# Performance work log

Measured on AMD Instinct MI355X. Metric: run time of the kernel, lower is better.

The kernel has to match this reference:

```python
import jax, jax.numpy as jnp
import numpy as np

B, L, D, H = 2, 2048, 768, 12
DH = D // H          # 64
DFF = 4 * D          # 3072
ALPHA = 0.25         # lorentz_alpha
BLEND = 0.5          # blend for FFN and MinkowskiLayerNorm (set via set_blend)
EPS = 1e-5
SCALE = float(np.sqrt(DH))


def setup_inputs() -> dict:
    key = jax.random.key(0)
    ks = jax.random.split(key, 14)
    w = lambda k, shape: jax.random.normal(k, shape, jnp.float32) * 0.02
    causal = jnp.tril(jnp.ones((L, L), bool))
    attention_mask = jnp.where(causal, 0.0, -1e9).astype(jnp.float32)[None, None]
    return {
        'x': jax.random.normal(ks[0], (B, L, D), jnp.float32),
        'attention_mask': attention_mask,
        'timelike_mask': jax.random.bernoulli(ks[1], 0.25, (D,)),
        'Wq': w(ks[2], (D, D)), 'Wk': w(ks[3], (D, D)),
        'Wv': w(ks[4], (D, D)), 'Wo': w(ks[5], (D, D)),
        'w1': w(ks[6], (DFF, D)), 'w2': w(ks[7], (D, DFF)),
        'w1_t': w(ks[8], (DFF // 2, D)), 'w2_t': w(ks[9], (D, DFF // 2)),
        'w1_s': w(ks[10], (DFF // 2, D)), 'w2_s': w(ks[11], (D, DFF // 2)),
        'n1_w': jnp.ones(D, jnp.float32), 'n1_b': jnp.zeros(D, jnp.float32),
        'n2_w': jnp.ones(D, jnp.float32), 'n2_b': jnp.zeros(D, jnp.float32),
    }


def _mink_norm(x, m, w, b):
    # Minkowski LayerNorm blended with standard LN (m: float timelike mask)
    mean = x.mean(-1, keepdims=True)
    xc = x - mean
    var = (xc * xc).mean(-1, keepdims=True)
    x_std = xc / jnp.sqrt(var + EPS)
    sq = xc * xc
    eta = (sq * (1.0 - m)).sum(-1, keepdims=True) - (sq * m).sum(-1, keepdims=True)
    x_eta = xc / jnp.sqrt(jnp.abs(eta) + EPS)
    xn = (1.0 - BLEND) * x_std + BLEND * x_eta
    return w * xn + b


def _attn(x, attention_mask, m, Wq, Wk, Wv, Wo):
    # (B,L,D) -> (B,H,L,DH)
    split = lambda t: t.reshape(B, L, H, DH).transpose(0, 2, 1, 3)
    Q = split(x @ Wq.T)
    K = split(x @ Wk.T)
    V = split(x @ Wv.T)
    scores = jnp.einsum('bhqd,bhkd->bhqk', Q, K) / SCALE
    # Minkowski timelike correction: per-head diagonal mask on Q
    m2 = m.reshape(H, DH)[None, :, None, :]          # (1,H,1,DH)
    Q_t = Q * m2
    q_norm = jnp.linalg.norm(Q, axis=-1, keepdims=True)
    qt_norm = jnp.linalg.norm(Q_t, axis=-1, keepdims=True)
    sf = jnp.where(qt_norm > 1e-6, q_norm / jnp.maximum(qt_norm, 1e-8), 0.0)
    time_inner = jnp.einsum('bhqd,bhkd->bhqk', Q_t * sf, K) / SCALE
    scores = scores - 2.0 * ALPHA * time_inner
    scores = scores + attention_mask
    aw = jax.nn.softmax(scores, axis=-1)
    out = jnp.einsum('bhqk,bhkd->bhqd', aw, V)
    out = out.transpose(0, 2, 1, 3).reshape(B, L, D)
    return out @ Wo.T


def _ffn(x, m, w1, w2, w1_t, w2_t, w1_s, w2_s):
    std_out = jax.nn.gelu(x @ w1.T, approximate=False) @ w2.T
    h_t = jax.nn.silu((x * m) @ w1_t.T) @ w2_t.T
    h_s = jax.nn.gelu((x * (1.0 - m)) @ w1_s.T, approximate=False) @ w2_s.T
    return (1.0 - BLEND) * std_out + BLEND * (h_t + h_s)


def reference(x, attention_mask, timelike_mask, Wq, Wk, Wv, Wo,
              w1, w2, w1_t, w2_t, w1_s, w2_s, n1_w, n1_b, n2_w, n2_b):
    m = timelike_mask.astype(jnp.float32)
    ao = _attn(_mink_norm(x, m, n1_w, n1_b), attention_mask, m, Wq, Wk, Wv, Wo)
    x = x + ao
    x = x + _ffn(_mink_norm(x, m, n2_w, n2_b), m, w1, w2, w1_t, w2_t, w1_s, w2_s)
    return x
```

## Files before the change

### kernel.cpp

```cpp
#include <hip/hip_runtime.h>


typedef unsigned short u16;
typedef __bf16 bfrag __attribute__((ext_vector_type(8)));
typedef float f32x4 __attribute__((ext_vector_type(4)));

#define MFMA(a, b, c) __builtin_amdgcn_mfma_f32_16x16x32_bf16(a, b, c, 0, 0, 0)
#define NEG_BIG (-30000.0f)
#define ASYNC16(g, l)                                                        \
  __builtin_amdgcn_global_load_lds(                                          \
      (const __attribute__((address_space(1))) unsigned int*)(g),            \
      (__attribute__((address_space(3))) unsigned int*)(l), 16, 0, 0)

__device__ __forceinline__ float bf2f(u16 u) {
  unsigned int v = ((unsigned int)u) << 16;
  float f; __builtin_memcpy(&f, &v, 4); return f;
}
__device__ __forceinline__ u16 f2bf(float f) {
  unsigned int v; __builtin_memcpy(&v, &f, 4);
  v += 0x7fffu + ((v >> 16) & 1u);
  return (u16)(v >> 16);
}
__device__ __forceinline__ bfrag ldfrag(const u16* p) {
  bfrag v; __builtin_memcpy(&v, p, 16); return v;
}

__device__ __forceinline__ int xcd_work_id() {
  const int nx = gridDim.x, ny = gridDim.y;
  const int nwg = nx * ny * gridDim.z;
  const int orig = blockIdx.x + nx * (blockIdx.y + ny * blockIdx.z);
  if (nwg & 7) return orig;
  return (orig & 7) * (nwg >> 3) + (orig >> 3);
}

__global__ __launch_bounds__(256) void mask_conv_k(const void* __restrict__ mask,
                                                   float* __restrict__ mfl) {
  __shared__ int msh;
  if (threadIdx.x == 0) msh = 0;
  __syncthreads();
  const unsigned int* w = (const unsigned int*)mask;
  if (threadIdx.x < 192) {
    const unsigned int v = w[threadIdx.x];
    if ((v & 0xFFFFu) == 0x3F80u) atomicOr(&msh, 4);
    else if (v == 0x3F800000u) atomicOr(&msh, 2);
    else if (v >= 2u) atomicOr(&msh, 1);
  }
  __syncthreads();
  const int m = msh;
  const int mode = (m & 4) ? 3 : (m & 2) ? 2 : (m & 1) ? 1 : 0;
  for (int i = threadIdx.x; i < 768; i += 256) {
    int b;
    if (mode == 3) b = ((const u16*)mask)[i] != 0;
    else if (mode == 2) b = ((const float*)mask)[i] != 0.0f;
    else if (mode == 1) b = ((const unsigned char*)mask)[i] != 0;
    else b = ((const int*)mask)[i] != 0;
    mfl[i] = (float)b;
  }
}

struct Segs {
  const void* src[14];
  int off[14];
  int n[14];
  int mmode[14];
};

__global__ __launch_bounds__(256) void convert_k(Segs segs, u16* __restrict__ dstb,
                                                 const float* __restrict__ mfl) {
  const int seg = blockIdx.y;
  const int n = segs.n[seg];
  const int mm = segs.mmode[seg];
  u16* dst = dstb + segs.off[seg];
  const float* src = (const float*)segs.src[seg];
  for (int i = (blockIdx.x * 256 + threadIdx.x) * 4; i < n; i += gridDim.x * 1024) {
    float4 v;
    __builtin_memcpy(&v, src + i, 16);
    if (mm) {
      const int k = i % 768;
      float m0 = mfl[k], m1 = mfl[k + 1], m2 = mfl[k + 2], m3 = mfl[k + 3];
      if (mm == 2) { m0 = 1.f - m0; m1 = 1.f - m1; m2 = 1.f - m2; m3 = 1.f - m3; }
      v.x *= m0; v.y *= m1; v.z *= m2; v.w *= m3;
    }
    dst[i] = f2bf(v.x); dst[i + 1] = f2bf(v.y);
    dst[i + 2] = f2bf(v.z); dst[i + 3] = f2bf(v.w);
  }
}

__global__ __launch_bounds__(256) void mink_norm_k(
    const float* __restrict__ X, const float* __restrict__ mf,
    const u16* __restrict__ w, const u16* __restrict__ bias,
    u16* __restrict__ Y, float* __restrict__ Xcopy) {
  __shared__ float red[8];
  const int row = blockIdx.x, tid = threadIdx.x;
  const int wid = tid >> 6, lane = tid & 63;
  const size_t roff = (size_t)row * 768;

  float xv[3], mv[3];
  int idx[3];
#pragma unroll
  for (int i = 0; i < 3; i++) {
    idx[i] = tid + i * 256;
    xv[i] = X[roff + idx[i]];
    mv[i] = mf[idx[i]];
  }
  if (Xcopy) {
#pragma unroll
    for (int i = 0; i < 3; i++) Xcopy[roff + idx[i]] = xv[i];
  }
  float s = xv[0] + xv[1] + xv[2];
#pragma unroll
  for (int o = 32; o >= 1; o >>= 1) s += __shfl_xor(s, o, 64);
  if (lane == 0) red[wid] = s;
  __syncthreads();
  const float mean = (red[0] + red[1] + red[2] + red[3]) * (1.0f / 768.0f);
  __syncthreads();

  float xc[3], ss = 0.0f, sm = 0.0f;
#pragma unroll
  for (int i = 0; i < 3; i++) {
    xc[i] = xv[i] - mean;
    ss += xc[i] * xc[i];
    sm += xc[i] * xc[i] * mv[i];
  }
#pragma unroll
  for (int o = 32; o >= 1; o >>= 1) {
    ss += __shfl_xor(ss, o, 64);
    sm += __shfl_xor(sm, o, 64);
  }
  if (lane == 0) { red[wid] = ss; red[4 + wid] = sm; }
  __syncthreads();
  const float sumsq = red[0] + red[1] + red[2] + red[3];
  const float summ = red[4] + red[5] + red[6] + red[7];
  const float var = sumsq * (1.0f / 768.0f);
  const float eta = sumsq - 2.0f * summ;
  const float rs = 1.0f / sqrtf(var + 1e-5f);
  const float re = 1.0f / sqrtf(fabsf(eta) + 1e-5f);

#pragma unroll
  for (int i = 0; i < 3; i++) {
    const float xn = xc[i] * 0.5f * (rs + re);
    Y[roff + idx[i]] = f2bf(bf2f(w[idx[i]]) * xn + bf2f(bias[idx[i]]));
  }
}

__global__ __launch_bounds__(256) void qcorr_k(u16* __restrict__ Q,
                                               const float* __restrict__ mf) {
  const int idx = blockIdx.x * 4 + (threadIdx.x >> 6);
  const int t = threadIdx.x & 63;
  const int h = idx % 12;
  const int bl = idx / 12;
  const size_t off = (size_t)bl * 768 + h * 64 + t;
  const float q = bf2f(Q[off]);
  const float m = mf[h * 64 + t];
  float q2 = q * q, qm2 = q * q * m;
#pragma unroll
  for (int o = 32; o >= 1; o >>= 1) {
    q2 += __shfl_xor(q2, o, 64);
    qm2 += __shfl_xor(qm2, o, 64);
  }
  const float qn = sqrtf(q2), qtn = sqrtf(qm2);
  const float sf = (qtn > 1e-6f) ? qn / fmaxf(qtn, 1e-8f) : 0.0f;
  Q[off] = f2bf(q * (1.0f - 0.5f * sf * m) * 0.125f);
}

__device__ __forceinline__ void gemm128_loop(
    const u16* __restrict__ Ab, const u16* __restrict__ Wb2,
    int K, int lda, int ldb, u16 (*As)[32], u16 (*Bs)[32], f32x4 acc[4][4]) {
  const int tid = threadIdx.x;
  const int wid = tid >> 6, lane = tid & 63;
  const int lr = lane & 15, lq = lane >> 4;
  const int srow = wid * 32 + (lane >> 2);
  const int scol = (lane & 3) * 8;
  const u16* ga0 = Ab + (size_t)srow * lda + scol;
  const u16* ga1 = Ab + (size_t)(srow + 16) * lda + scol;
  const u16* gb0 = Wb2 + (size_t)srow * ldb + scol;
  const u16* gb1 = Wb2 + (size_t)(srow + 16) * ldb + scol;
  const int wr = (wid >> 1) * 64, wc = (wid & 1) * 64;
  const int nt = K >> 5;

#define STAGE16(dbuf, k0)                                                    \
  {                                                                          \
    u16* _a0 = &As[(dbuf) * 128 + wid * 32][0];                              \
    u16* _a1 = &As[(dbuf) * 128 + wid * 32 + 16][0];                         \
    u16* _b0 = &Bs[(dbuf) * 128 + wid * 32][0];                              \
    u16* _b1 = &Bs[(dbuf) * 128 + wid * 32 + 16][0];                         \
    ASYNC16(ga0 + (k0), _a0);                                                \
    ASYNC16(ga1 + (k0), _a1);                                                \
    ASYNC16(gb0 + (k0), _b0);                                                \
    ASYNC16(gb1 + (k0), _b1);                                                \
  }

  STAGE16(0, 0);
  for (int t = 0; t < nt; ++t) {
    const int cur = t & 1;
    if (t + 1 < nt) {
      STAGE16(cur ^ 1, (t + 1) << 5);
      __builtin_amdgcn_sched_barrier(0);
      asm volatile("s_waitcnt vmcnt(4)" ::: "memory");
    } else {
      asm volatile("s_waitcnt vmcnt(0)" ::: "memory");
    }
    __builtin_amdgcn_s_barrier();
    __builtin_amdgcn_sched_barrier(0);
    bfrag af[4], bf4[4];
#pragma unroll
    for (int i = 0; i < 4; i++)
      af[i] = ldfrag(&As[cur * 128 + wr + i * 16 + lr][lq * 8]);
#pragma unroll
    for (int j = 0; j < 4; j++)
      bf4[j] = ldfrag(&Bs[cur * 128 + wc + j * 16 + lr][lq * 8]);
#pragma unroll
    for (int i = 0; i < 4; i++)
#pragma unroll
      for (int j = 0; j < 4; j++)
        acc[i][j] = MFMA(af[i], bf4[j], acc[i][j]);
    asm volatile("s_waitcnt lgkmcnt(0)" ::: "memory");
    __builtin_amdgcn_sched_barrier(0);
    __builtin_amdgcn_s_barrier();
  }
#undef STAGE16
}

struct GSeg { const u16* W; u16* C; int ldc; int nblk; int epi; };
struct GArgs { GSeg s[3]; };

__global__ __launch_bounds__(256) void gemm128_fused(
    const u16* __restrict__ A, int lda, int K, GArgs args) {
  __shared__ __align__(16) u16 As[256][32];
  __shared__ __align__(16) u16 Bs[256][32];
  const int w = xcd_work_id();
  int cb = w % gridDim.x, seg = 0;
  const int by = w / gridDim.x;
  while (cb >= args.s[seg].nblk) { cb -= args.s[seg].nblk; seg++; }
  const GSeg g = args.s[seg];
  const int rowb = by * 128, colb = cb * 128;
  f32x4 acc[4][4] = {};
  gemm128_loop(A + (size_t)rowb * lda, g.W + (size_t)colb * K, K, lda, K,
               As, Bs, acc);

  const int lane = threadIdx.x & 63, wid = threadIdx.x >> 6;
  const int lr = lane & 15, lq = lane >> 4;
  const int wr = (wid >> 1) * 64, wc = (wid & 1) * 64;
#pragma unroll
  for (int i = 0; i < 4; i++)
#pragma unroll
    for (int j = 0; j < 4; j++)
#pragma unroll
      for (int r = 0; r < 4; r++) {
        const int row = rowb + wr + i * 16 + lq * 4 + r;
        const int col = colb + wc + j * 16 + lr;
        float v = acc[i][j][r];
        if (g.epi == 2) v = 0.5f * v * (1.0f + erff(v * 0.70710678118654752f));
        else if (g.epi == 3) v = v / (1.0f + __expf(-v));
        g.C[(size_t)row * g.ldc + col] = f2bf(v);
      }
}

__global__ __launch_bounds__(256) void gemm128_wo_splitk(
    const u16* __restrict__ A, const u16* __restrict__ W,
    float* __restrict__ Out) {
  __shared__ __align__(16) u16 As[256][32];
  __shared__ __align__(16) u16 Bs[256][32];
  const int w = xcd_work_id();
  const int bx = w % gridDim.x;
  const int by = (w / gridDim.x) % gridDim.y;
  const int z = w / (gridDim.x * gridDim.y);
  const int rowb = by * 128, colb = bx * 128;
  f32x4 acc[4][4] = {};
  gemm128_loop(A + (size_t)rowb * 768 + z * 384,
               W + (size_t)colb * 768 + z * 384, 384, 768, 768, As, Bs, acc);

  const int lane = threadIdx.x & 63, wid = threadIdx.x >> 6;
  const int lr = lane & 15, lq = lane >> 4;
  const int wr = (wid >> 1) * 64, wc = (wid & 1) * 64;
#pragma unroll
  for (int i = 0; i < 4; i++)
#pragma unroll
    for (int j = 0; j < 4; j++)
#pragma unroll
      for (int r = 0; r < 4; r++) {
        const int row = rowb + wr + i * 16 + lq * 4 + r;
        const int col = colb + wc + j * 16 + lr;
        atomicAdd(&Out[(size_t)row * 768 + col], acc[i][j][r]);
      }
}

__global__ __launch_bounds__(256) void ffn2_splitk(
    const u16* __restrict__ H1, const u16* __restrict__ Ht,
    const u16* __restrict__ Hs, const u16* __restrict__ W2,
    const u16* __restrict__ W2t, const u16* __restrict__ W2s,
    float* __restrict__ Out) {
  __shared__ __align__(16) u16 As[256][32];
  __shared__ __align__(16) u16 Bs[256][32];
  const int w = xcd_work_id();
  const int bx = w % gridDim.x;
  const int by = (w / gridDim.x) % gridDim.y;
  const int z = w / (gridDim.x * gridDim.y);
  const int rowb = by * 128, colb = bx * 128;
  f32x4 acc[4][4] = {};
  if (z == 0)
    gemm128_loop(H1 + (size_t)rowb * 3072, W2 + (size_t)colb * 3072,
                 1536, 3072, 3072, As, Bs, acc);
  else if (z == 1)
    gemm128_loop(H1 + (size_t)rowb * 3072 + 1536,
                 W2 + (size_t)colb * 3072 + 1536,
                 1536, 3072, 3072, As, Bs, acc);
  else if (z == 2)
    gemm128_loop(Ht + (size_t)rowb * 1536, W2t + (size_t)colb * 1536,
                 1536, 1536, 1536, As, Bs, acc);
  else
    gemm128_loop(Hs + (size_t)rowb * 1536, W2s + (size_t)colb * 1536,
                 1536, 1536, 1536, As, Bs, acc);

  const int lane = threadIdx.x & 63, wid = threadIdx.x >> 6;
  const int lr = lane & 15, lq = lane >> 4;
  const int wr = (wid >> 1) * 64, wc = (wid & 1) * 64;
#pragma unroll
  for (int i = 0; i < 4; i++)
#pragma unroll
    for (int j = 0; j < 4; j++)
#pragma unroll
      for (int r = 0; r < 4; r++) {
        const int row = rowb + wr + i * 16 + lq * 4 + r;
        const int col = colb + wc + j * 16 + lr;
        atomicAdd(&Out[(size_t)row * 768 + col], 0.5f * acc[i][j][r]);
      }
}

__global__ __launch_bounds__(256) void flash_attn_k(
    const u16* __restrict__ Qc, const u16* __restrict__ Kb,
    const u16* __restrict__ Vb, u16* __restrict__ O,
    float* __restrict__ Pn, float* __restrict__ Ph) {
  __shared__ __align__(16) u16 Ks[64][40];
  __shared__ __align__(16) u16 Vt[64][72];
  __shared__ __align__(16) u16 Ps[4][16][72];
  const int tid = threadIdx.x, wid = tid >> 6, lane = tid & 63;
  const int lr = lane & 15, lq = lane >> 4;

  int bx = blockIdx.x, qt = 0, c = 0;
  for (int q = 31; q >= 0; --q) {
    const int nc = (q < 8) ? 1 : (q / 8 + 1);
    if (bx < nc) { qt = q; c = bx; break; }
    bx -= nc;
  }
  const int nt = qt + 1;
  const int t0 = c * 8;
  const int t1 = (t0 + 8 < nt) ? t0 + 8 : nt;

  const int qb = qt * 64;
  const int bh = blockIdx.y;
  const int b = bh / 12, h = bh % 12;
  const int q0 = qb + wid * 16;
  const size_t base = (size_t)b * 2048 * 768 + h * 64;

  bfrag aq[2];
  aq[0] = ldfrag(Qc + base + (size_t)(q0 + lr) * 768 + lq * 8);
  aq[1] = ldfrag(Qc + base + (size_t)(q0 + lr) * 768 + 32 + lq * 8);

  f32x4 o[4] = {};
  float mrow[4] = {NEG_BIG, NEG_BIG, NEG_BIG, NEG_BIG};
  float lrow[4] = {0.0f, 0.0f, 0.0f, 0.0f};

  const int krow = tid >> 3;
  const int kcol = (tid & 7) * 8;
  const int vkey = tid & 31;
  const int vdg = tid >> 5;

  const u16* kp = Kb + base + (size_t)(t0 * 64 + krow) * 768 + kcol;
  const u16* vp = Vb + base + (size_t)(t0 * 64 + vkey) * 768 + vdg * 8;

  uint4 kv0, kv1, vv0, vv1;
  __builtin_memcpy(&kv0, kp, 16);
  __builtin_memcpy(&kv1, kp + (size_t)32 * 768, 16);
  __builtin_memcpy(&vv0, vp, 16);
  __builtin_memcpy(&vv1, vp + (size_t)32 * 768, 16);

  for (int kt = t0; kt < t1; kt++) {
    __syncthreads();
    __builtin_memcpy(&Ks[krow][kcol], &kv0, 16);
    __builtin_memcpy(&Ks[krow + 32][kcol], &kv1, 16);
    {
      union { uint4 u; u16 s[8]; } a, b2;
      a.u = vv0; b2.u = vv1;
#pragma unroll
      for (int j = 0; j < 8; j++) {
        Vt[vdg * 8 + j][vkey] = a.s[j];
        Vt[vdg * 8 + j][vkey + 32] = b2.s[j];
      }
    }
    __syncthreads();
    if (kt + 1 < t1) {
      const size_t koff = (size_t)(kt + 1 - t0) * 64 * 768;
      __builtin_memcpy(&kv0, kp + koff, 16);
      __builtin_memcpy(&kv1, kp + koff + (size_t)32 * 768, 16);
      __builtin_memcpy(&vv0, vp + koff, 16);
      __builtin_memcpy(&vv1, vp + koff + (size_t)32 * 768, 16);
    }

    const int kbk = kt * 64;
    {
      f32x4 s4[4] = {};
#pragma unroll
      for (int kg = 0; kg < 2; kg++) {
#pragma unroll
        for (int cc = 0; cc < 4; cc++) {
          bfrag bk = ldfrag(&Ks[cc * 16 + lr][kg * 32 + lq * 8]);
          s4[cc] = MFMA(aq[kg], bk, s4[cc]);
        }
      }
#pragma unroll
      for (int r = 0; r < 4; r++) {
        const int q = q0 + lq * 4 + r;
        float v[4];
        float mx = NEG_BIG;
#pragma unroll
        for (int cc = 0; cc < 4; cc++) {
          v[cc] = (kbk + cc * 16 + lr > q) ? NEG_BIG : s4[cc][r];
          mx = fmaxf(mx, v[cc]);
        }
#pragma unroll
        for (int off = 8; off >= 1; off >>= 1)
          mx = fmaxf(mx, __shfl_xor(mx, off, 16));
        const float mn = fmaxf(mrow[r], mx);
        const float alpha = __expf(mrow[r] - mn);
        float sm = 0.0f;
        float p[4];
#pragma unroll
        for (int cc = 0; cc < 4; cc++) {
          p[cc] = __expf(v[cc] - mn);
          sm += p[cc];
        }
#pragma unroll
        for (int off = 8; off >= 1; off >>= 1) sm += __shfl_xor(sm, off, 16);
        lrow[r] = lrow[r] * alpha + sm;
        mrow[r] = mn;
#pragma unroll
        for (int dt = 0; dt < 4; dt++) o[dt][r] *= alpha;
#pragma unroll
        for (int cc = 0; cc < 4; cc++)
          Ps[wid][lq * 4 + r][cc * 16 + lr] = f2bf(p[cc]);
      }
      __threadfence_block();
      bfrag pf0 = ldfrag(&Ps[wid][lr][lq * 8]);
      bfrag pf1 = ldfrag(&Ps[wid][lr][32 + lq * 8]);
#pragma unroll
      for (int dt = 0; dt < 4; dt++) {
        bfrag v0 = ldfrag(&Vt[dt * 16 + lr][lq * 8]);
        bfrag v1 = ldfrag(&Vt[dt * 16 + lr][32 + lq * 8]);
        o[dt] = MFMA(pf0, v0, o[dt]);
        o[dt] = MFMA(pf1, v1, o[dt]);
      }
    }
  }

  if (qt < 8) {
#pragma unroll
    for (int r = 0; r < 4; r++) {
      const float inv = 1.0f / fmaxf(lrow[r], 1e-30f);
      const int q = q0 + lq * 4 + r;
#pragma unroll
      for (int dt = 0; dt < 4; dt++)
        O[base + (size_t)q * 768 + dt * 16 + lr] = f2bf(o[dt][r] * inv);
    }
  } else {
    int off = 0;
    for (int j = 8; j < qt; ++j) off += j / 8 + 1;
    const int s = bh * 72 + off + c;
    float* Op = (s < 1536) ? Pn + (size_t)s * 4096
                           : Ph + (size_t)(s - 1536) * 4096;
    float* lmp = Ph + 786432 + (size_t)s * 128;
#pragma unroll
    for (int r = 0; r < 4; r++) {
      const int row = wid * 16 + lq * 4 + r;
#pragma unroll
      for (int dt = 0; dt < 4; dt++)
        Op[(size_t)row * 64 + dt * 16 + lr] = o[dt][r];
      if (lr == 0) { lmp[row] = mrow[r]; lmp[64 + row] = lrow[r]; }
    }
  }
}

__global__ __launch_bounds__(256) void attn_merge_k(
    const float* __restrict__ Pn, const float* __restrict__ Ph,
    u16* __restrict__ O) {
  const int qt = 8 + blockIdx.x;
  const int bh = blockIdx.y;
  const int b = bh / 12, h = bh % 12;
  const int nc = qt / 8 + 1;
  int off = 0;
  for (int j = 8; j < qt; ++j) off += j / 8 + 1;
  const int s0 = bh * 72 + off;
  const int row = threadIdx.x >> 2;
  const int c0 = (threadIdx.x & 3) * 16;
  const float* lmb = Ph + 786432;

  float mg = NEG_BIG;
  for (int cc = 0; cc < nc; ++cc)
    mg = fmaxf(mg, lmb[(size_t)(s0 + cc) * 128 + row]);

  float acc[16];
#pragma unroll
  for (int j = 0; j < 16; j++) acc[j] = 0.0f;
  float lg = 0.0f;
  for (int cc = 0; cc < nc; ++cc) {
    const int s = s0 + cc;
    const float mcv = lmb[(size_t)s * 128 + row];
    const float coef = __expf(mcv - mg);
    lg += coef * lmb[(size_t)s * 128 + 64 + row];
    const float* Op = (s < 1536) ? Pn + (size_t)s * 4096
                                 : Ph + (size_t)(s - 1536) * 4096;
    const float* rp = Op + (size_t)row * 64 + c0;
#pragma unroll
    for (int g = 0; g < 4; g++) {
      float4 v;
      __builtin_memcpy(&v, rp + g * 4, 16);
      acc[g * 4 + 0] += coef * v.x;
      acc[g * 4 + 1] += coef * v.y;
      acc[g * 4 + 2] += coef * v.z;
      acc[g * 4 + 3] += coef * v.w;
    }
  }
  const float inv = 1.0f / fmaxf(lg, 1e-30f);
  const int q = qt * 64 + row;
  const size_t ob = (size_t)b * 2048 * 768 + h * 64 + (size_t)q * 768 + c0;
#pragma unroll
  for (int j = 0; j < 16; j++) O[ob + j] = f2bf(acc[j] * inv);
}

extern "C" void kernel_launch(void* const* d_in, const int* in_sizes, int n_in,
                              void* d_out, int out_size, void* d_ws,
                              size_t ws_size, hipStream_t stream) {
  (void)in_sizes; (void)n_in; (void)out_size; (void)ws_size;
  const float* x = (const float*)d_in[0];
  const void* mask = d_in[2];

  char* ws = (char*)d_ws;
  u16* Wb  = (u16*)(ws);
  u16* n1h = (u16*)(ws + 23599104);
  u16* Qb  = (u16*)(ws + 48764928);
  u16* Kb2 = (u16*)(ws + 55056384);
  u16* Vb2 = (u16*)(ws + 61347840);
  u16* att = (u16*)(ws + 67639296);
  u16* hs  = (u16*)(ws + 80222208);
  float* mfl = (float*)(ws + 92805120);
  float* x1 = (float*)d_out;
  float* Pn = (float*)n1h;
  float* Ph = (float*)hs;

  u16* Wq = Wb + 0,        *Wk = Wb + 589824,   *Wv = Wb + 1179648;
  u16* Wo = Wb + 1769472,  *w1 = Wb + 2359296,  *w1t = Wb + 4718592;
  u16* w1s = Wb + 5898240, *w2 = Wb + 7077888,  *w2t = Wb + 9437184;
  u16* w2s = Wb + 10616832;
  u16* n1w = Wb + 11796480, *n1b = Wb + 11797248;
  u16* n2w = Wb + 11798016, *n2b = Wb + 11798784;

  Segs sg;
  const int srcidx[14] = {3, 4, 5, 6, 7, 9, 11, 8, 10, 12, 13, 14, 15, 16};
  const int offs[14] = {0, 589824, 1179648, 1769472, 2359296, 4718592,
                        5898240, 7077888, 9437184, 10616832,
                        11796480, 11797248, 11798016, 11798784};
  const int ns[14] = {589824, 589824, 589824, 589824, 2359296, 1179648,
                      1179648, 2359296, 1179648, 1179648, 768, 768, 768, 768};
  const int mms[14] = {0, 0, 0, 0, 0, 1, 2, 0, 0, 0, 0, 0, 0, 0};
  for (int i = 0; i < 14; i++) {
    sg.src[i] = d_in[srcidx[i]];
    sg.off[i] = offs[i];
    sg.n[i] = ns[i];
    sg.mmode[i] = mms[i];
  }

  mask_conv_k<<<1, 256, 0, stream>>>(mask, mfl);
  convert_k<<<dim3(2304, 14), 256, 0, stream>>>(sg, Wb, mfl);

  mink_norm_k<<<4096, 256, 0, stream>>>(x, mfl, n1w, n1b, n1h, x1);

  GArgs qkv;
  qkv.s[0] = {Wq, Qb, 768, 6, 0};
  qkv.s[1] = {Wk, Kb2, 768, 6, 0};
  qkv.s[2] = {Wv, Vb2, 768, 6, 0};
  gemm128_fused<<<dim3(18, 32), 256, 0, stream>>>(n1h, 768, 768, qkv);

  qcorr_k<<<12288, 256, 0, stream>>>(Qb, mfl);

  flash_attn_k<<<dim3(80, 24), 256, 0, stream>>>(Qb, Kb2, Vb2, att, Pn, Ph);
  attn_merge_k<<<dim3(24, 24), 256, 0, stream>>>(Pn, Ph, att);

  gemm128_wo_splitk<<<dim3(6, 32, 2), 256, 0, stream>>>(att, Wo, x1);

  mink_norm_k<<<4096, 256, 0, stream>>>(x1, mfl, n2w, n2b, Qb, nullptr);

  GArgs ffn1;
  ffn1.s[0] = {w1, n1h, 3072, 24, 2};
  ffn1.s[1] = {w1t, att, 1536, 12, 3};
  ffn1.s[2] = {w1s, hs, 1536, 12, 2};
  gemm128_fused<<<dim3(48, 32), 256, 0, stream>>>(Qb, 768, 768, ffn1);

  ffn2_splitk<<<dim3(6, 32, 4), 256, 0, stream>>>(n1h, att, hs, w2, w2t, w2s,
                                                  (float*)d_out);
}
```

Measured before the change: 424.2 us.

## Replace atomic split-K FFN2 with three-way partial buffers and a reduce kernel

The second FFN GEMM now uses a three-way split instead of four. The standard branch runs its full K=3072 and updates the output in place without atomics. The timelike and spacelike branches write their partials to scratch buffers, one in fp32 and one in bf16, and a new elementwise kernel adds them into the output. This removes roughly twelve million fp32 atomicAdds and remaps block order across XCDs. In exchange, the z=0 blocks do twice the K work of the others, so the load is uneven, and there is an extra kernel launch. Rounding the spacelike partial to bf16 also adds some error.

```diff
diff --git a/kernel.cpp b/kernel.cpp
--- a/kernel.cpp
+++ b/kernel.cpp
@@ -285,27 +285,24 @@
       }
 }
 
-__global__ __launch_bounds__(256) void ffn2_splitk(
+__global__ __launch_bounds__(256) void ffn2_split3(
     const u16* __restrict__ H1, const u16* __restrict__ Ht,
     const u16* __restrict__ Hs, const u16* __restrict__ W2,
     const u16* __restrict__ W2t, const u16* __restrict__ W2s,
-    float* __restrict__ Out) {
+    float* __restrict__ Out, float* __restrict__ Pt, u16* __restrict__ Ps16) {
   __shared__ __align__(16) u16 As[256][32];
   __shared__ __align__(16) u16 Bs[256][32];
-  const int w = xcd_work_id();
-  const int bx = w % gridDim.x;
-  const int by = (w / gridDim.x) % gridDim.y;
-  const int z = w / (gridDim.x * gridDim.y);
+  const int orig = blockIdx.x + 6 * (blockIdx.y + 32 * blockIdx.z);
+  const int w = (orig & 7) * 72 + (orig >> 3);
+  const int z = w % 3;
+  const int bx = (w / 3) % 6;
+  const int by = w / 18;
   const int rowb = by * 128, colb = bx * 128;
   f32x4 acc[4][4] = {};
   if (z == 0)
     gemm128_loop(H1 + (size_t)rowb * 3072, W2 + (size_t)colb * 3072,
-                 1536, 3072, 3072, As, Bs, acc);
+                 3072, 3072, 3072, As, Bs, acc);
   else if (z == 1)
-    gemm128_loop(H1 + (size_t)rowb * 3072 + 1536,
-                 W2 + (size_t)colb * 3072 + 1536,
-                 1536, 3072, 3072, As, Bs, acc);
-  else if (z == 2)
     gemm128_loop(Ht + (size_t)rowb * 1536, W2t + (size_t)colb * 1536,
                  1536, 1536, 1536, As, Bs, acc);
   else
@@ -323,8 +320,27 @@
       for (int r = 0; r < 4; r++) {
         const int row = rowb + wr + i * 16 + lq * 4 + r;
         const int col = colb + wc + j * 16 + lr;
-        atomicAdd(&Out[(size_t)row * 768 + col], 0.5f * acc[i][j][r]);
+        const size_t o = (size_t)row * 768 + col;
+        if (z == 0) Out[o] = Out[o] + 0.5f * acc[i][j][r];
+        else if (z == 1) Pt[o] = acc[i][j][r];
+        else Ps16[o] = f2bf(acc[i][j][r]);
       }
+}
+
+__global__ __launch_bounds__(256) void ffn2_reduce(
+    float* __restrict__ Out, const float* __restrict__ Pt,
+    const u16* __restrict__ Ps16) {
+  const int i = (blockIdx.x * 256 + threadIdx.x) * 4;
+  float4 o, t;
+  __builtin_memcpy(&o, Out + i, 16);
+  __builtin_memcpy(&t, Pt + i, 16);
+  ushort4 s;
+  __builtin_memcpy(&s, Ps16 + i, 8);
+  o.x += 0.5f * (t.x + bf2f(s.x));
+  o.y += 0.5f * (t.y + bf2f(s.y));
+  o.z += 0.5f * (t.z + bf2f(s.z));
+  o.w += 0.5f * (t.w + bf2f(s.w));
+  __builtin_memcpy(Out + i, &o, 16);
 }
 
 __global__ __launch_bounds__(256) void flash_attn_k(
@@ -546,6 +562,8 @@
   float* x1 = (float*)d_out;
   float* Pn = (float*)n1h;
   float* Ph = (float*)hs;
+  float* Pt = (float*)Qb;
+  u16* Ps16 = Vb2;
 
   u16* Wq = Wb + 0,        *Wk = Wb + 589824,   *Wv = Wb + 1179648;
   u16* Wo = Wb + 1769472,  *w1 = Wb + 2359296,  *w1t = Wb + 4718592;
@@ -595,6 +613,7 @@
   ffn1.s[2] = {w1s, hs, 1536, 12, 2};
   gemm128_fused<<<dim3(48, 32), 256, 0, stream>>>(Qb, 768, 768, ffn1);
 
-  ffn2_splitk<<<dim3(6, 32, 4), 256, 0, stream>>>(n1h, att, hs, w2, w2t, w2s,
-                                                  (float*)d_out);
-}
+  ffn2_split3<<<dim3(6, 32, 3), 256, 0, stream>>>(n1h, att, hs, w2, w2t, w2s,
+                                                  (float*)d_out, Pt, Ps16);
+  ffn2_reduce<<<3072, 256, 0, stream>>>((float*)d_out, Pt, Ps16);
+}
```

Result: slower. 438.2 us (+3.3%).

## Fuse Q timelike correction into QKV GEMM epilogue, finer attention split with fp16 partials

Applied to the files above, without the earlier changes.

Drops the separate qcorr kernel and instead computes the per-head Q norm and timelike-norm correction inside the QKV GEMM epilogue, using cross-lane shuffles over the 64-column head slice each wave owns. The flash attention split-KV chunk size goes from 8 to 4 KV tiles, which raises the block count and balances load across the causal triangle. Partial outputs are now stored as fp16 instead of fp32, with the max and sum statistics moved to a separate buffer. The fp16 partials halve the merge traffic but lose some precision, and the smaller chunks mean more partials to write and merge.

```diff
diff --git a/kernel.cpp b/kernel.cpp
--- a/kernel.cpp
+++ b/kernel.cpp
@@ -20,6 +20,12 @@
   unsigned int v; __builtin_memcpy(&v, &f, 4);
   v += 0x7fffu + ((v >> 16) & 1u);
   return (u16)(v >> 16);
+}
+__device__ __forceinline__ u16 f2h(float f) {
+  _Float16 h = (_Float16)f; u16 u; __builtin_memcpy(&u, &h, 2); return u;
+}
+__device__ __forceinline__ float h2f(u16 u) {
+  _Float16 h; __builtin_memcpy(&h, &u, 2); return (float)h;
 }
 __device__ __forceinline__ bfrag ldfrag(const u16* p) {
   bfrag v; __builtin_memcpy(&v, p, 16); return v;
@@ -143,26 +149,6 @@
   }
 }
 
-__global__ __launch_bounds__(256) void qcorr_k(u16* __restrict__ Q,
-                                               const float* __restrict__ mf) {
-  const int idx = blockIdx.x * 4 + (threadIdx.x >> 6);
-  const int t = threadIdx.x & 63;
-  const int h = idx % 12;
-  const int bl = idx / 12;
-  const size_t off = (size_t)bl * 768 + h * 64 + t;
-  const float q = bf2f(Q[off]);
-  const float m = mf[h * 64 + t];
-  float q2 = q * q, qm2 = q * q * m;
-#pragma unroll
-  for (int o = 32; o >= 1; o >>= 1) {
-    q2 += __shfl_xor(q2, o, 64);
-    qm2 += __shfl_xor(qm2, o, 64);
-  }
-  const float qn = sqrtf(q2), qtn = sqrtf(qm2);
-  const float sf = (qtn > 1e-6f) ? qn / fmaxf(qtn, 1e-8f) : 0.0f;
-  Q[off] = f2bf(q * (1.0f - 0.5f * sf * m) * 0.125f);
-}
-
 __device__ __forceinline__ void gemm128_loop(
     const u16* __restrict__ Ab, const u16* __restrict__ Wb2,
     int K, int lda, int ldb, u16 (*As)[32], u16 (*Bs)[32], f32x4 acc[4][4]) {
@@ -225,7 +211,8 @@
 struct GArgs { GSeg s[3]; };
 
 __global__ __launch_bounds__(256) void gemm128_fused(
-    const u16* __restrict__ A, int lda, int K, GArgs args) {
+    const u16* __restrict__ A, int lda, int K, GArgs args,
+    const float* __restrict__ mfl) {
   __shared__ __align__(16) u16 As[256][32];
   __shared__ __align__(16) u16 Bs[256][32];
   const int w = xcd_work_id();
@@ -241,6 +228,41 @@
   const int lane = threadIdx.x & 63, wid = threadIdx.x >> 6;
   const int lr = lane & 15, lq = lane >> 4;
   const int wr = (wid >> 1) * 64, wc = (wid & 1) * 64;
+
+  if (g.epi == 1) {
+    const int cb64 = colb + wc;
+    float mj[4];
+#pragma unroll
+    for (int j = 0; j < 4; j++) mj[j] = mfl[cb64 + j * 16 + lr];
+#pragma unroll
+    for (int i = 0; i < 4; i++)
+#pragma unroll
+      for (int r = 0; r < 4; r++) {
+        float p2 = 0.0f, pm2 = 0.0f;
+#pragma unroll
+        for (int j = 0; j < 4; j++) {
+          const float v = acc[i][j][r];
+          p2 += v * v;
+          pm2 += v * v * mj[j];
+        }
+#pragma unroll
+        for (int off = 8; off >= 1; off >>= 1) {
+          p2 += __shfl_xor(p2, off, 64);
+          pm2 += __shfl_xor(pm2, off, 64);
+        }
+        const float qn = sqrtf(p2), qtn = sqrtf(pm2);
+        const float sf = (qtn > 1e-6f) ? qn / fmaxf(qtn, 1e-8f) : 0.0f;
+        const int row = rowb + wr + i * 16 + lq * 4 + r;
+#pragma unroll
+        for (int j = 0; j < 4; j++) {
+          const int col = cb64 + j * 16 + lr;
+          const float v = acc[i][j][r] * (1.0f - 0.5f * sf * mj[j]) * 0.125f;
+          g.C[(size_t)row * g.ldc + col] = f2bf(v);
+        }
+      }
+    return;
+  }
+
 #pragma unroll
   for (int i = 0; i < 4; i++)
 #pragma unroll
@@ -330,7 +352,7 @@
 __global__ __launch_bounds__(256) void flash_attn_k(
     const u16* __restrict__ Qc, const u16* __restrict__ Kb,
     const u16* __restrict__ Vb, u16* __restrict__ O,
-    float* __restrict__ Pn, float* __restrict__ Ph) {
+    u16* __restrict__ Pn, u16* __restrict__ Ph, float* __restrict__ Lm) {
   __shared__ __align__(16) u16 Ks[64][40];
   __shared__ __align__(16) u16 Vt[64][72];
   __shared__ __align__(16) u16 Ps[4][16][72];
@@ -339,13 +361,13 @@
 
   int bx = blockIdx.x, qt = 0, c = 0;
   for (int q = 31; q >= 0; --q) {
-    const int nc = (q < 8) ? 1 : (q / 8 + 1);
+    const int nc = (q < 4) ? 1 : (q / 4 + 1);
     if (bx < nc) { qt = q; c = bx; break; }
     bx -= nc;
   }
   const int nt = qt + 1;
-  const int t0 = c * 8;
-  const int t1 = (t0 + 8 < nt) ? t0 + 8 : nt;
+  const int t0 = c * 4;
+  const int t1 = (t0 + 4 < nt) ? t0 + 4 : nt;
 
   const int qb = qt * 64;
   const int bh = blockIdx.y;
@@ -453,7 +475,7 @@
     }
   }
 
-  if (qt < 8) {
+  if (qt < 4) {
 #pragma unroll
     for (int r = 0; r < 4; r++) {
       const float inv = 1.0f / fmaxf(lrow[r], 1e-30f);
@@ -464,39 +486,38 @@
     }
   } else {
     int off = 0;
-    for (int j = 8; j < qt; ++j) off += j / 8 + 1;
-    const int s = bh * 72 + off + c;
-    float* Op = (s < 1536) ? Pn + (size_t)s * 4096
-                           : Ph + (size_t)(s - 1536) * 4096;
-    float* lmp = Ph + 786432 + (size_t)s * 128;
+    for (int j = 4; j < qt; ++j) off += j / 4 + 1;
+    const int s = bh * 140 + off + c;
+    u16* Op = (s < 3072) ? Pn + (size_t)s * 4096
+                         : Ph + (size_t)(s - 3072) * 4096;
+    float* lmp = Lm + (size_t)s * 128;
 #pragma unroll
     for (int r = 0; r < 4; r++) {
       const int row = wid * 16 + lq * 4 + r;
 #pragma unroll
       for (int dt = 0; dt < 4; dt++)
-        Op[(size_t)row * 64 + dt * 16 + lr] = o[dt][r];
+        Op[(size_t)row * 64 + dt * 16 + lr] = f2h(o[dt][r]);
       if (lr == 0) { lmp[row] = mrow[r]; lmp[64 + row] = lrow[r]; }
     }
   }
 }
 
 __global__ __launch_bounds__(256) void attn_merge_k(
-    const float* __restrict__ Pn, const float* __restrict__ Ph,
-    u16* __restrict__ O) {
-  const int qt = 8 + blockIdx.x;
+    const u16* __restrict__ Pn, const u16* __restrict__ Ph,
+    const float* __restrict__ Lm, u16* __restrict__ O) {
+  const int qt = 4 + blockIdx.x;
   const int bh = blockIdx.y;
   const int b = bh / 12, h = bh % 12;
-  const int nc = qt / 8 + 1;
+  const int nc = qt / 4 + 1;
   int off = 0;
-  for (int j = 8; j < qt; ++j) off += j / 8 + 1;
-  const int s0 = bh * 72 + off;
+  for (int j = 4; j < qt; ++j) off += j / 4 + 1;
+  const int s0 = bh * 140 + off;
   const int row = threadIdx.x >> 2;
   const int c0 = (threadIdx.x & 3) * 16;
-  const float* lmb = Ph + 786432;
 
   float mg = NEG_BIG;
   for (int cc = 0; cc < nc; ++cc)
-    mg = fmaxf(mg, lmb[(size_t)(s0 + cc) * 128 + row]);
+    mg = fmaxf(mg, Lm[(size_t)(s0 + cc) * 128 + row]);
 
   float acc[16];
 #pragma unroll
@@ -504,21 +525,16 @@
   float lg = 0.0f;
   for (int cc = 0; cc < nc; ++cc) {
     const int s = s0 + cc;
-    const float mcv = lmb[(size_t)s * 128 + row];
+    const float mcv = Lm[(size_t)s * 128 + row];
     const float coef = __expf(mcv - mg);
-    lg += coef * lmb[(size_t)s * 128 + 64 + row];
-    const float* Op = (s < 1536) ? Pn + (size_t)s * 4096
-                                 : Ph + (size_t)(s - 1536) * 4096;
-    const float* rp = Op + (size_t)row * 64 + c0;
-#pragma unroll
-    for (int g = 0; g < 4; g++) {
-      float4 v;
-      __builtin_memcpy(&v, rp + g * 4, 16);
-      acc[g * 4 + 0] += coef * v.x;
-      acc[g * 4 + 1] += coef * v.y;
-      acc[g * 4 + 2] += coef * v.z;
-      acc[g * 4 + 3] += coef * v.w;
-    }
+    lg += coef * Lm[(size_t)s * 128 + 64 + row];
+    const u16* Op = (s < 3072) ? Pn + (size_t)s * 4096
+                               : Ph + (size_t)(s - 3072) * 4096;
+    const u16* rp = Op + (size_t)row * 64 + c0;
+    u16 tv[16];
+    __builtin_memcpy(tv, rp, 32);
+#pragma unroll
+    for (int j = 0; j < 16; j++) acc[j] += coef * h2f(tv[j]);
   }
   const float inv = 1.0f / fmaxf(lg, 1e-30f);
   const int q = qt * 64 + row;
@@ -544,8 +560,9 @@
   u16* hs  = (u16*)(ws + 80222208);
   float* mfl = (float*)(ws + 92805120);
   float* x1 = (float*)d_out;
-  float* Pn = (float*)n1h;
-  float* Ph = (float*)hs;
+  u16* Pn16 = n1h;
+  u16* Ph16 = hs;
+  float* Lm = (float*)(ws + 80222208 + 4194304);
 
   u16* Wq = Wb + 0,        *Wk = Wb + 589824,   *Wv = Wb + 1179648;
   u16* Wo = Wb + 1769472,  *w1 = Wb + 2359296,  *w1t = Wb + 4718592;
@@ -575,15 +592,14 @@
   mink_norm_k<<<4096, 256, 0, stream>>>(x, mfl, n1w, n1b, n1h, x1);
 
   GArgs qkv;
-  qkv.s[0] = {Wq, Qb, 768, 6, 0};
+  qkv.s[0] = {Wq, Qb, 768, 6, 1};
   qkv.s[1] = {Wk, Kb2, 768, 6, 0};
   qkv.s[2] = {Wv, Vb2, 768, 6, 0};
-  gemm128_fused<<<dim3(18, 32), 256, 0, stream>>>(n1h, 768, 768, qkv);
-
-  qcorr_k<<<12288, 256, 0, stream>>>(Qb, mfl);
-
-  flash_attn_k<<<dim3(80, 24), 256, 0, stream>>>(Qb, Kb2, Vb2, att, Pn, Ph);
-  attn_merge_k<<<dim3(24, 24), 256, 0, stream>>>(Pn, Ph, att);
+  gemm128_fused<<<dim3(18, 32), 256, 0, stream>>>(n1h, 768, 768, qkv, mfl);
+
+  flash_attn_k<<<dim3(144, 24), 256, 0, stream>>>(Qb, Kb2, Vb2, att,
+                                                  Pn16, Ph16, Lm);
+  attn_merge_k<<<dim3(28, 24), 256, 0, stream>>>(Pn16, Ph16, Lm, att);
 
   gemm128_wo_splitk<<<dim3(6, 32, 2), 256, 0, stream>>>(att, Wo, x1);
 
@@ -593,7 +609,7 @@
   ffn1.s[0] = {w1, n1h, 3072, 24, 2};
   ffn1.s[1] = {w1t, att, 1536, 12, 3};
   ffn1.s[2] = {w1s, hs, 1536, 12, 2};
-  gemm128_fused<<<dim3(48, 32), 256, 0, stream>>>(Qb, 768, 768, ffn1);
+  gemm128_fused<<<dim3(48, 32), 256, 0, stream>>>(Qb, 768, 768, ffn1, mfl);
 
   ffn2_splitk<<<dim3(6, 32, 4), 256, 0, stream>>>(n1h, att, hs, w2, w2t, w2s,
                                                   (float*)d_out);
```

After: 411.3 us. 1.03x faster.
